# Performance work log

Measured on AMD Instinct MI355X. Metric: run time of the kernel, lower is better.

Reference implementation:

```python
import jax, jax.numpy as jnp
import numpy as np

B = 512          # graphs
NODES = 90       # nodes per graph (fixed by lin1 = Linear(90*L*H, ...))
N = B * NODES    # total nodes
F_IN = 90        # dataset.num_features
H = 128          # hidden
L = 3            # num_layers
HL = 64          # hidden_linear
C = 2            # dataset.num_classes
DEG = 16         # avg degree
E = N * DEG      # total edges


def setup_inputs() -> dict:
    key = jax.random.key(0)
    ks = jax.random.split(key, 14)
    x = jax.random.normal(ks[0], (N, F_IN), jnp.float32)
    # intra-graph random edges: graph g owns nodes [g*90, (g+1)*90)
    g = jnp.repeat(jnp.arange(B), NODES * DEG)
    src = g * NODES + jax.random.randint(ks[1], (E,), 0, NODES)
    dst = g * NODES + jax.random.randint(ks[2], (E,), 0, NODES)
    edge_index = jnp.stack([src, dst]).astype(jnp.int64)
    edge_attr = jax.random.uniform(ks[3], (E,), jnp.float32, 0.1, 1.0)
    batch = jnp.repeat(jnp.arange(B), NODES).astype(jnp.int64)

    def lin(k, fi, fo):
        s = 1.0 / np.sqrt(fi)
        kw, kb = jax.random.split(k)
        return (jax.random.uniform(kw, (fi, fo), jnp.float32, -s, s),
                jax.random.uniform(kb, (fo,), jnp.float32, -s, s))

    W1, b1 = lin(ks[4], F_IN, H)
    W2, b2 = lin(ks[5], H, H)
    W3, b3 = lin(ks[6], H, H)
    lin1_W, lin1_b = lin(ks[7], NODES * L * H, HL)
    lin2_W, lin2_b = lin(ks[8], HL, C)
    return {"x": x, "edge_attr": edge_attr, "W1": W1, "b1": b1, "W2": W2,
            "b2": b2, "W3": W3, "b3": b3, "lin1_W": lin1_W, "lin1_b": lin1_b,
            "lin2_W": lin2_W, "lin2_b": lin2_b, "edge_index": edge_index,
            "batch": batch}


def reference(x, edge_attr, W1, b1, W2, b2, W3, b3, lin1_W, lin1_b,
              lin2_W, lin2_b, edge_index, batch):
    src, dst = edge_index[0], edge_index[1]
    # GCN normalization with added self-loops (weight 1), as in PyG GCNConv
    loop = jnp.arange(N)
    s = jnp.concatenate([src, loop])
    d = jnp.concatenate([dst, loop])
    w = jnp.concatenate([edge_attr, jnp.ones((N,), x.dtype)])
    deg = jax.ops.segment_sum(w, d, num_segments=N)
    dis = jnp.where(deg > 0, jax.lax.rsqrt(jnp.maximum(deg, 1e-30)), 0.0)
    norm = dis[s] * w * dis[d]  # [E+N]

    def conv(h, W, b):
        h = h @ W                                  # [N, H]
        msg = norm[:, None] * h[s]                 # gather+scale [E+N, H]
        return jax.ops.segment_sum(msg, d, num_segments=N) + b

    h1 = jax.nn.relu(conv(x, W1, b1))
    h2 = jax.nn.relu(conv(h1, W2, b2))
    h3 = jax.nn.relu(conv(h2, W3, b3))
    xc = jnp.concatenate([h1, h2, h3], axis=1)     # [N, L*H]
    # to_dense_batch: every graph has exactly 90 nodes in order, so no padding
    # (fill_value never appears) and dense batching is a pure reshape.
    z = xc.reshape(B, NODES * L * H)
    h = jax.nn.relu(z @ lin1_W + lin1_b)
    logits = h @ lin2_W + lin2_b                   # dropout is identity in eval
    return jax.nn.log_softmax(logits, axis=-1)
```

## Files before the change

### kernel.cpp

```cpp
#include <hip/hip_runtime.h>

typedef __bf16 bfx8 __attribute__((ext_vector_type(8)));
typedef float fx4 __attribute__((ext_vector_type(4)));
typedef unsigned short us4 __attribute__((ext_vector_type(4)));
typedef unsigned short us8 __attribute__((ext_vector_type(8)));

#define NNODES 90
#define NPAD   96
#define HF     128
#define NGRAPH 512
#define EPG    1440
#define ETOT   (NGRAPH*EPG)
#define KTOT   34560
#define NKTOT  1080
#define KSPLIT 45
#define KSTEPS (NKTOT/KSPLIT)

__device__ __forceinline__ unsigned short f2bf(float f){
  union { float f; unsigned u; } v; v.f = f;
  return (unsigned short)((v.u + 0x7FFFu + ((v.u>>16)&1u)) >> 16);
}
__device__ __forceinline__ int hsw(int node, int f){
  return node*HF + ((((f>>3) ^ (node&15)))<<3) + (f&7);
}

__global__ __launch_bounds__(256) void pack_all_kern(
    const float* __restrict__ W1,
    const float* __restrict__ W2,
    const float* __restrict__ W3,
    const float* __restrict__ L1W,
    unsigned short* __restrict__ o1,
    unsigned short* __restrict__ o2,
    unsigned short* __restrict__ o3,
    unsigned short* __restrict__ l1p,
    float* __restrict__ accf)
{
  __shared__ __align__(16) unsigned short tile[32*64];
  int b = blockIdx.x;
  int t = threadIdx.x;
  if (b < NKTOT) {
    int ks = b;
#pragma unroll
    for (int j=0;j<8;j++) tile[t*8+j] = f2bf(L1W[ks*32*64 + t*8 + j]);
    __syncthreads();
    int lane = t & 63;
    int nt = t >> 6;
    int n  = nt*16 + (lane&15);
    int kq = (lane>>4)*8;
    us8 v;
#pragma unroll
    for (int j=0;j<8;j++) v[j] = tile[(kq+j)*64 + n];
    *(us8*)&l1p[((nt*NKTOT + ks)*64 + lane)*8] = v;
  } else if (b < NKTOT + 22) {
    int bb = b - NKTOT;
    const float* W; unsigned short* out; int K, nK, tt;
    if (bb < 6)       { W = W1; out = o1; K = 90;  nK = 3; tt = bb*256 + t; }
    else if (bb < 14) { W = W2; out = o2; K = 128; nK = 4; tt = (bb-6)*256 + t; }
    else              { W = W3; out = o3; K = 128; nK = 4; tt = (bb-14)*256 + t; }
    int lane = tt & 63;
    int ks = (tt>>6) % nK;
    int nt = (tt>>6) / nK;
    int n  = nt*16 + (lane&15);
    int k0 = ks*32 + (lane>>4)*8;
    unsigned short v[8];
#pragma unroll
    for (int j=0;j<8;j++){ int k=k0+j; v[j] = (k<K)? f2bf(W[k*128+n]) : (unsigned short)0; }
    unsigned short* o = out + ((nt*nK+ks)*64 + lane)*8;
#pragma unroll
    for (int j=0;j<8;j++) o[j]=v[j];
  } else {
    int base = (b - (NKTOT+22))*16384 + t*4;
#pragma unroll
    for (int i = 0; i < 16; ++i) {
      fx4 z = {0.f,0.f,0.f,0.f};
      *(fx4*)&accf[base + i*1024] = z;
    }
  }
}

__global__ __launch_bounds__(512) void gcn_layers_kern(
    const float* __restrict__ x,
    const float* __restrict__ eattr,
    const int* __restrict__ ei,
    const unsigned short* __restrict__ w1p,
    const unsigned short* __restrict__ w2p,
    const unsigned short* __restrict__ w3p,
    const float* __restrict__ b1,
    const float* __restrict__ b2,
    const float* __restrict__ b3,
    unsigned short* __restrict__ xc)
{
  __shared__ __align__(16) char smem[65280];
  unsigned short* Abf = (unsigned short*)smem;
  unsigned short* H   = (unsigned short*)(smem + 17280);
  unsigned short* Tt  = (unsigned short*)(smem + 40320);
  float* Af  = (float*)(smem + 17280);
  float* deg = (float*)(smem + 64896);

  const int g = blockIdx.x;
  const int tid = threadIdx.x;
  const int lane = tid & 63, wave = tid >> 6;
  const int q = lane >> 4, r = lane & 15;
  const int eb = g*EPG;
  const int nb = g*NNODES;
  const long long* e64 = (const long long*)ei;

  bool i64f;
  {
    int v = ei[2*lane + 1];
    i64f = (__ballot(v != 0) == 0ull);
  }

  const int e0 = tid, e1 = tid + 512, e2 = tid + 1024;
  const bool h2 = (e2 < EPG);
  int s0, d0, s1, d1, s2 = nb, d2 = nb;
  if (i64f) {
    s0 = (int)e64[eb+e0]; d0 = (int)e64[ETOT+eb+e0];
    s1 = (int)e64[eb+e1]; d1 = (int)e64[ETOT+eb+e1];
    if (h2) { s2 = (int)e64[eb+e2]; d2 = (int)e64[ETOT+eb+e2]; }
  } else {
    s0 = ei[eb+e0]; d0 = ei[ETOT+eb+e0];
    s1 = ei[eb+e1]; d1 = ei[ETOT+eb+e1];
    if (h2) { s2 = ei[eb+e2]; d2 = ei[ETOT+eb+e2]; }
  }
  float w0 = eattr[eb+e0];
  float w1 = eattr[eb+e1];
  float w2 = h2 ? eattr[eb+e2] : 0.f;

  for (int i = tid; i < NPAD; i += 512) deg[i] = 1.0f;
  for (int i = tid; i < NNODES*NPAD; i += 512) Af[i] = 0.0f;
  __syncthreads();
  atomicAdd(&Af[(d0-nb)*NPAD + (s0-nb)], w0); atomicAdd(&deg[d0-nb], w0);
  atomicAdd(&Af[(d1-nb)*NPAD + (s1-nb)], w1); atomicAdd(&deg[d1-nb], w1);
  if (h2) { atomicAdd(&Af[(d2-nb)*NPAD + (s2-nb)], w2); atomicAdd(&deg[d2-nb], w2); }
  __syncthreads();
  for (int i = tid; i < NPAD; i += 512) deg[i] = rsqrtf(deg[i]);
  __syncthreads();
  for (int i = tid; i < NNODES*NPAD; i += 512) {
    int row = i / NPAD, col = i - row*NPAD;
    float a = Af[i];
    if (col == row) a += 1.0f;
    Abf[i] = f2bf(a * deg[row] * deg[col]);
  }
  __syncthreads();
  for (int i = tid; i < NNODES*90; i += 512) {
    int node = i/90, f = i - node*90;
    H[hsw(node, f)] = f2bf(x[(nb + node)*90 + f]);
  }
  for (int i = tid; i < NNODES*6; i += 512) {
    int node = i/6, f = 90 + (i - node*6);
    H[hsw(node, f)] = 0;
  }
  __syncthreads();

#pragma unroll
  for (int l = 0; l < 3; ++l) {
    const unsigned short* wpk = (l==0)? w1p : (l==1)? w2p : w3p;
    const float* bias         = (l==0)? b1 : (l==1)? b2 : b3;
    const int nK = (l==0)? 3 : 4;

    bfx8 wf[4];
#pragma unroll
    for (int ks = 0; ks < 4; ++ks)
      if (ks < nK) wf[ks] = *(const bfx8*)(const void*)&wpk[((wave*nK + ks)*64 + lane)*8];

    for (int mt = 0; mt < 6; ++mt) {
      int row = mt*16 + r; if (row > 89) row = 89;
      fx4 acc = {0.f,0.f,0.f,0.f};
#pragma unroll
      for (int ks = 0; ks < 4; ++ks)
        if (ks < nK) {
          bfx8 af = *(const bfx8*)(const void*)&H[row*HF + (((4*ks + q) ^ (row&15))<<3)];
          acc = __builtin_amdgcn_mfma_f32_16x16x32_bf16(af, wf[ks], acc, 0,0,0);
        }
      us4 o;
#pragma unroll
      for (int i2=0;i2<4;i2++) o[i2] = f2bf(acc[i2]);
      *(us4*)&Tt[(wave*16 + r)*NPAD + mt*16 + q*4] = o;
    }
    __syncthreads();

    {
      bfx8 tf[3];
#pragma unroll
      for (int ks = 0; ks < 3; ++ks)
        tf[ks] = *(const bfx8*)(const void*)&Tt[(wave*16 + r)*NPAD + ks*32 + q*8];
      float bv[4];
#pragma unroll
      for (int i2=0;i2<4;i2++) bv[i2] = bias[wave*16 + q*4 + i2];
      for (int nt = 0; nt < 6; ++nt) {
        int arow = nt*16 + r; if (arow > 89) arow = 89;
        fx4 acc = {0.f,0.f,0.f,0.f};
#pragma unroll
        for (int ks = 0; ks < 3; ++ks) {
          bfx8 bfr = *(const bfx8*)(const void*)&Abf[arow*NPAD + ks*32 + q*8];
          acc = __builtin_amdgcn_mfma_f32_16x16x32_bf16(tf[ks], bfr, acc, 0,0,0);
        }
        int m = nt*16 + r;
        if (m < NNODES) {
          us4 o;
#pragma unroll
          for (int i2=0;i2<4;i2++){
            float v = acc[i2] + bv[i2];
            o[i2] = f2bf(v > 0.f ? v : 0.f);
          }
          *(us4*)&H[m*HF + (((2*wave + (q>>1)) ^ (m&15))<<3) + (q&1)*4] = o;
        }
      }
    }
    __syncthreads();

    for (int i = tid*4; i < NNODES*HF; i += 512*4) {
      int node = i >> 7, f = i & 127;
      us4 v = *(const us4*)&H[node*HF + (((f>>3) ^ (node&15))<<3) + (f&7)];
      *(us4*)&xc[(nb + node)*384 + l*128 + f] = v;
    }
  }
}

__global__ __launch_bounds__(256) void gemm2_kern(
    const unsigned short* __restrict__ z,
    const unsigned short* __restrict__ wp,
    float* __restrict__ accf)
{
  __shared__ __align__(16) unsigned short zt[32*128];
  int mb = blockIdx.x % 16;
  int kb = blockIdx.x / 16;
  int tid = threadIdx.x;
  int lane = tid & 63, wave = tid >> 6;
  int q = lane >> 4, r = lane & 15;
  int mt = wave >> 1;
  int nt0 = (wave & 1)*2;
  int m0 = mb*32;

  fx4 acc0 = {0,0,0,0}, acc1 = {0,0,0,0};
  int Lm = tid >> 3, Lc = tid & 7;
  int cA = Lc ^ (Lm & 7);
  int arow = mt*16 + r;
  const unsigned short* zrow = &z[(m0+Lm)*KTOT];

  us8 pvA = *(const us8*)&zrow[kb*KSTEPS*32 + cA*8];
  us8 pvB = *(const us8*)&zrow[kb*KSTEPS*32 + (cA+8)*8];

  for (int it = 0; it < KSTEPS/4; ++it) {
    *(us8*)&zt[Lm*128 + Lc*8] = pvA;
    *(us8*)&zt[Lm*128 + (Lc+8)*8] = pvB;
    __syncthreads();
    if (it < KSTEPS/4 - 1) {
      int kn = (kb*KSTEPS + (it+1)*4)*32;
      pvA = *(const us8*)&zrow[kn + cA*8];
      pvB = *(const us8*)&zrow[kn + (cA+8)*8];
    }
    int ks0 = kb*KSTEPS + it*4;
#pragma unroll
    for (int ks2 = 0; ks2 < 4; ++ks2) {
      int c = ks2*4 + q;
      int pos = (c & 8) | ((c & 7) ^ (arow & 7));
      bfx8 af = *(const bfx8*)(const void*)&zt[arow*128 + pos*8];
      int ksg = ks0 + ks2;
      bfx8 bA = *(const bfx8*)(const void*)&wp[(((nt0+0)*NKTOT + ksg)*64 + lane)*8];
      bfx8 bB = *(const bfx8*)(const void*)&wp[(((nt0+1)*NKTOT + ksg)*64 + lane)*8];
      acc0 = __builtin_amdgcn_mfma_f32_16x16x32_bf16(af, bA, acc0, 0,0,0);
      acc1 = __builtin_amdgcn_mfma_f32_16x16x32_bf16(af, bB, acc1, 0,0,0);
    }
    __syncthreads();
  }
#pragma unroll
  for (int i2 = 0; i2 < 4; ++i2) {
    int row = m0 + mt*16 + q*4 + i2;
    atomicAdd(&accf[row*64 + (nt0+0)*16 + r], acc0[i2]);
    atomicAdd(&accf[row*64 + (nt0+1)*16 + r], acc1[i2]);
  }
}

__global__ __launch_bounds__(256) void head_kern(
    const float* __restrict__ accf,
    const float* __restrict__ l1b,
    const float* __restrict__ l2w,
    const float* __restrict__ l2b,
    float* __restrict__ out)
{
  int gph = blockIdx.x*4 + (threadIdx.x >> 6);
  int j = threadIdx.x & 63;
  float h = accf[gph*64 + j] + l1b[j];
  h = h > 0.f ? h : 0.f;
  float p0 = h * l2w[2*j];
  float p1 = h * l2w[2*j+1];
  for (int off = 32; off; off >>= 1) {
    p0 += __shfl_down(p0, off);
    p1 += __shfl_down(p1, off);
  }
  if (j == 0) {
    float l0 = p0 + l2b[0];
    float l1 = p1 + l2b[1];
    float mx = fmaxf(l0, l1);
    float lse = mx + logf(expf(l0-mx) + expf(l1-mx));
    out[gph*2]   = l0 - lse;
    out[gph*2+1] = l1 - lse;
  }
}

extern "C" void kernel_launch(void* const* d_in, const int* in_sizes, int n_in,
                              void* d_out, int out_size, void* d_ws, size_t ws_size,
                              hipStream_t stream)
{
  const float* x   = (const float*)d_in[0];
  const float* ea  = (const float*)d_in[1];
  const float* W1  = (const float*)d_in[2];
  const float* b1  = (const float*)d_in[3];
  const float* W2  = (const float*)d_in[4];
  const float* b2  = (const float*)d_in[5];
  const float* W3  = (const float*)d_in[6];
  const float* b3  = (const float*)d_in[7];
  const float* L1W = (const float*)d_in[8];
  const float* L1b = (const float*)d_in[9];
  const float* L2W = (const float*)d_in[10];
  const float* L2b = (const float*)d_in[11];
  const int* ei    = (const int*)d_in[12];
  float* out       = (float*)d_out;

  char* ws = (char*)d_ws;
  unsigned short* xc  = (unsigned short*)(ws);
  unsigned short* l1p = (unsigned short*)(ws + 35389440);
  unsigned short* w1p = (unsigned short*)(ws + 39813120);
  unsigned short* w2p = (unsigned short*)(ws + 39837696);
  unsigned short* w3p = (unsigned short*)(ws + 39870464);
  float* accf         = (float*)(ws + 39903232);

  pack_all_kern<<<NKTOT + 22 + 2, 256, 0, stream>>>(W1, W2, W3, L1W,
                                                    w1p, w2p, w3p, l1p, accf);
  gcn_layers_kern<<<NGRAPH, 512, 0, stream>>>(x, ea, ei, w1p, w2p, w3p,
                                              b1, b2, b3, xc);
  gemm2_kern<<<16*KSPLIT, 256, 0, stream>>>(xc, l1p, accf);
  head_kern<<<NGRAPH/4, 256, 0, stream>>>(accf, L1b, L2W, L2b, out);
}
```

Measured before the change: 143.9 us.

## Compute degrees by row reduction, vectorize xc copy, drop LDS staging in gemm2

The GCN kernel no longer does separate atomic adds for degrees. Each node's degree is now a shuffle-reduced row sum of the dense adjacency tile, and Af is zeroed with 16-byte stores. The xc write-out reads 8 contiguous bf16 values from the swizzled H tile and un-swizzles the destination address. The gemm2 kernel drops its shared-memory staging and barriers for the z operand, so each lane loads its MFMA A fragment straight from global memory in an unrolled loop. That last step trades LDS reuse and coalesced loads for fewer syncs, and may raise global traffic or cut coalescing on z.

```diff
diff --git a/kernel.cpp b/kernel.cpp
--- a/kernel.cpp
+++ b/kernel.cpp
@@ -127,14 +127,30 @@
   float w1 = eattr[eb+e1];
   float w2 = h2 ? eattr[eb+e2] : 0.f;
 
-  for (int i = tid; i < NPAD; i += 512) deg[i] = 1.0f;
-  for (int i = tid; i < NNODES*NPAD; i += 512) Af[i] = 0.0f;
-  __syncthreads();
-  atomicAdd(&Af[(d0-nb)*NPAD + (s0-nb)], w0); atomicAdd(&deg[d0-nb], w0);
-  atomicAdd(&Af[(d1-nb)*NPAD + (s1-nb)], w1); atomicAdd(&deg[d1-nb], w1);
-  if (h2) { atomicAdd(&Af[(d2-nb)*NPAD + (s2-nb)], w2); atomicAdd(&deg[d2-nb], w2); }
-  __syncthreads();
-  for (int i = tid; i < NPAD; i += 512) deg[i] = rsqrtf(deg[i]);
+  for (int i = tid*4; i < NNODES*NPAD; i += 512*4) {
+    fx4 zv = {0.f,0.f,0.f,0.f};
+    *(fx4*)&Af[i] = zv;
+  }
+  __syncthreads();
+  atomicAdd(&Af[(d0-nb)*NPAD + (s0-nb)], w0);
+  atomicAdd(&Af[(d1-nb)*NPAD + (s1-nb)], w1);
+  if (h2) atomicAdd(&Af[(d2-nb)*NPAD + (s2-nb)], w2);
+  __syncthreads();
+  {
+    int l16 = tid & 15;
+    for (int row = tid >> 4; row < NPAD; row += 32) {
+      float s = 0.f;
+      if (row < NNODES) {
+#pragma unroll
+        for (int j = 0; j < 6; ++j) s += Af[row*NPAD + l16 + 16*j];
+      }
+      s += __shfl_xor(s, 1);
+      s += __shfl_xor(s, 2);
+      s += __shfl_xor(s, 4);
+      s += __shfl_xor(s, 8);
+      if (l16 == 0) deg[row] = (row < NNODES) ? rsqrtf(1.f + s) : 1.0f;
+    }
+  }
   __syncthreads();
   for (int i = tid; i < NNODES*NPAD; i += 512) {
     int row = i / NPAD, col = i - row*NPAD;
@@ -210,10 +226,11 @@
     }
     __syncthreads();
 
-    for (int i = tid*4; i < NNODES*HF; i += 512*4) {
-      int node = i >> 7, f = i & 127;
-      us4 v = *(const us4*)&H[node*HF + (((f>>3) ^ (node&15))<<3) + (f&7)];
-      *(us4*)&xc[(nb + node)*384 + l*128 + f] = v;
+    for (int i = tid*8; i < NNODES*HF; i += 512*8) {
+      int node = i >> 7, p = (i >> 3) & 15;
+      us8 v = *(const us8*)&H[i];
+      int f0 = (p ^ (node&15)) << 3;
+      *(us8*)&xc[(nb + node)*384 + l*128 + f0] = v;
     }
   }
 }
@@ -223,7 +240,6 @@
     const unsigned short* __restrict__ wp,
     float* __restrict__ accf)
 {
-  __shared__ __align__(16) unsigned short zt[32*128];
   int mb = blockIdx.x % 16;
   int kb = blockIdx.x / 16;
   int tid = threadIdx.x;
@@ -233,37 +249,18 @@
   int nt0 = (wave & 1)*2;
   int m0 = mb*32;
 
+  const unsigned short* zbase = &z[(m0 + mt*16 + r)*KTOT + (kb*KSTEPS)*32 + q*8];
+  const unsigned short* wb0   = &wp[((nt0+0)*NKTOT + kb*KSTEPS)*512 + lane*8];
+  const unsigned short* wb1   = &wp[((nt0+1)*NKTOT + kb*KSTEPS)*512 + lane*8];
+
   fx4 acc0 = {0,0,0,0}, acc1 = {0,0,0,0};
-  int Lm = tid >> 3, Lc = tid & 7;
-  int cA = Lc ^ (Lm & 7);
-  int arow = mt*16 + r;
-  const unsigned short* zrow = &z[(m0+Lm)*KTOT];
-
-  us8 pvA = *(const us8*)&zrow[kb*KSTEPS*32 + cA*8];
-  us8 pvB = *(const us8*)&zrow[kb*KSTEPS*32 + (cA+8)*8];
-
-  for (int it = 0; it < KSTEPS/4; ++it) {
-    *(us8*)&zt[Lm*128 + Lc*8] = pvA;
-    *(us8*)&zt[Lm*128 + (Lc+8)*8] = pvB;
-    __syncthreads();
-    if (it < KSTEPS/4 - 1) {
-      int kn = (kb*KSTEPS + (it+1)*4)*32;
-      pvA = *(const us8*)&zrow[kn + cA*8];
-      pvB = *(const us8*)&zrow[kn + (cA+8)*8];
-    }
-    int ks0 = kb*KSTEPS + it*4;
-#pragma unroll
-    for (int ks2 = 0; ks2 < 4; ++ks2) {
-      int c = ks2*4 + q;
-      int pos = (c & 8) | ((c & 7) ^ (arow & 7));
-      bfx8 af = *(const bfx8*)(const void*)&zt[arow*128 + pos*8];
-      int ksg = ks0 + ks2;
-      bfx8 bA = *(const bfx8*)(const void*)&wp[(((nt0+0)*NKTOT + ksg)*64 + lane)*8];
-      bfx8 bB = *(const bfx8*)(const void*)&wp[(((nt0+1)*NKTOT + ksg)*64 + lane)*8];
-      acc0 = __builtin_amdgcn_mfma_f32_16x16x32_bf16(af, bA, acc0, 0,0,0);
-      acc1 = __builtin_amdgcn_mfma_f32_16x16x32_bf16(af, bB, acc1, 0,0,0);
-    }
-    __syncthreads();
+#pragma unroll 4
+  for (int it = 0; it < KSTEPS; ++it) {
+    bfx8 af = *(const bfx8*)(const void*)&zbase[it*32];
+    bfx8 bA = *(const bfx8*)(const void*)&wb0[it*512];
+    bfx8 bB = *(const bfx8*)(const void*)&wb1[it*512];
+    acc0 = __builtin_amdgcn_mfma_f32_16x16x32_bf16(af, bA, acc0, 0,0,0);
+    acc1 = __builtin_amdgcn_mfma_f32_16x16x32_bf16(af, bB, acc1, 0,0,0);
   }
 #pragma unroll
   for (int i2 = 0; i2 < 4; ++i2) {
```

New measurement: 144.4 us. About the same (+0.3%).
